# Performance work log

Hardware: AMD Instinct MI355X
Metric: run time of the kernel (lower is better)

Reference implementation:

```python
import jax, jax.numpy as jnp
import numpy as np

NUM_HEADS = 16

def _rmsnorm(x, w):
    eps = jnp.finfo(x.dtype).eps  # torch nn.RMSNorm default eps
    ms = jnp.mean(x * x, axis=-1, keepdims=True)
    return x * jax.lax.rsqrt(ms + eps) * w

def _heads(x):
    B, S, D = x.shape
    return x.reshape(B, S, NUM_HEADS, D // NUM_HEADS)

def _attn(q, k, v):
    # q:[B,Sq,H,D] k,v:[B,Sk,H,D]; non-causal softmax attention
    scale = 1.0 / np.sqrt(q.shape[-1]).astype(np.float32)
    s = jnp.einsum('bqhd,bkhd->bhqk', q, k) * scale
    p = jax.nn.softmax(s, axis=-1)
    return jnp.einsum('bhqk,bkhd->bqhd', p, v)

def _gate(ctx, W1, b1, W2, b2):
    # Linear -> SiLU -> Linear(dim->1) -> sigmoid ; returns [B,S,1]
    h = jax.nn.silu(ctx @ W1.T + b1)
    return jax.nn.sigmoid(h @ W2.T + b2)

def setup_inputs() -> dict:
    key = jax.random.key(0)
    ks = jax.random.split(key, 20)
    B, Sq, Sk, St, dim = 4, 512, 2048, 512, 1024
    n = lambda k, shp, s=1.0: jax.random.normal(k, shp, jnp.float32) * s
    W = lambda k, o, i: n(k, (o, i), 0.02)
    return {
        'queries': n(ks[0], (B, Sq, dim)),
        'context_visual': n(ks[1], (B, Sk, dim)),
        'context_text': n(ks[2], (B, St, dim)),
        'w_norm_q': jnp.ones((dim,), jnp.float32),
        'w_norm_v': jnp.ones((dim,), jnp.float32),
        'w_norm_t': jnp.ones((dim,), jnp.float32),
        'Wq': W(ks[3], dim, dim), 'bq': n(ks[4], (dim,), 0.02),
        'Wk_vis': W(ks[5], dim, dim), 'bk_vis': jnp.zeros((dim,), jnp.float32),
        'Wv_vis': W(ks[6], dim, dim), 'bv_vis': jnp.zeros((dim,), jnp.float32),
        'Wk_text': W(ks[7], dim, dim), 'bk_text': jnp.zeros((dim,), jnp.float32),
        'Wv_text': W(ks[8], dim, dim), 'bv_text': jnp.zeros((dim,), jnp.float32),
        'Wg1v': W(ks[9], dim, dim), 'bg1v': jnp.zeros((dim,), jnp.float32),
        'Wg2v': W(ks[10], 1, dim), 'bg2v': jnp.zeros((1,), jnp.float32),
        'Wg1t': W(ks[11], dim, dim), 'bg1t': jnp.zeros((dim,), jnp.float32),
        'Wg2t': W(ks[12], 1, dim), 'bg2t': jnp.zeros((1,), jnp.float32),
        'Wo': W(ks[13], dim, dim), 'bo': jnp.zeros((dim,), jnp.float32),
    }

def reference(queries, context_visual, context_text,
              w_norm_q, w_norm_v, w_norm_t,
              Wq, bq, Wk_vis, bk_vis, Wv_vis, bv_vis,
              Wk_text, bk_text, Wv_text, bv_text,
              Wg1v, bg1v, Wg2v, bg2v, Wg1t, bg1t, Wg2t, bg2t,
              Wo, bo):
    residual = queries
    qn = _rmsnorm(queries, w_norm_q)
    cv = _rmsnorm(context_visual, w_norm_v)
    ct = _rmsnorm(context_text, w_norm_t)
    q = _heads(qn @ Wq.T + bq)
    k_vis = _heads(cv @ Wk_vis.T + bk_vis)
    v_vis = _heads(cv @ Wv_vis.T + bv_vis)
    v_vis = v_vis * _gate(cv, Wg1v, bg1v, Wg2v, bg2v)[..., None]  # [B,Sk,1,1]
    h = _attn(q, k_vis, v_vis)
    k_text = _heads(ct @ Wk_text.T + bk_text)
    v_text = _heads(ct @ Wv_text.T + bv_text)
    v_text = v_text * _gate(ct, Wg1t, bg1t, Wg2t, bg2t)[..., None]
    h = h + _attn(q, k_text, v_text)
    B, Sq, H, D = h.shape
    out = h.reshape(B, Sq, H * D) @ Wo.T + bo  # dropout p=0 -> identity
    return residual + out
```

## Files before the change

kernel.cpp:

```cpp
#include <hip/hip_runtime.h>
#include <hip/hip_bf16.h>

typedef __attribute__((ext_vector_type(4))) float f32x4;
typedef __attribute__((ext_vector_type(8))) short s16x8;
typedef __attribute__((ext_vector_type(4))) short s16x4;
using bf16 = __hip_bfloat16;

static constexpr int BB  = 4;
static constexpr int SQ  = 512;
static constexpr int SKV = 2048;
static constexpr int SKT = 512;
static constexpr int DIM = 1024;
static constexpr int NH  = 16;
static constexpr int HD  = 64;

#define MFMA32(A,B,C) __builtin_amdgcn_mfma_f32_16x16x32_bf16(A,B,C,0,0,0)

#if __has_builtin(__builtin_amdgcn_mfma_f32_16x16x16_bf16)
  #define MFMA16(A,B,C) __builtin_amdgcn_mfma_f32_16x16x16_bf16(A,B,C,0,0,0)
  #define HAVE_X16 1
#elif __has_builtin(__builtin_amdgcn_mfma_f32_16x16x16bf16_1k)
  #define MFMA16(A,B,C) __builtin_amdgcn_mfma_f32_16x16x16bf16_1k(A,B,C,0,0,0)
  #define HAVE_X16 1
#else
  #define HAVE_X16 0
#endif

#define SBAR() asm volatile("s_barrier" ::: "memory")

__device__ __forceinline__ float b2f(short s) {
  unsigned int u = ((unsigned int)(unsigned short)s) << 16;
  float f; __builtin_memcpy(&f, &u, 4); return f;
}
__device__ __forceinline__ short f2s(float f) {
  bf16 h = __float2bfloat16(f); short s; __builtin_memcpy(&s, &h, 2); return s;
}

__device__ __forceinline__ void gload16(const void* g, void* l) {
  __builtin_amdgcn_global_load_lds(
      (const __attribute__((address_space(1))) void*)g,
      (__attribute__((address_space(3))) void*)l, 16, 0, 0);
}

static constexpr float QSCALE = 0.180336880111120426f;

struct CastArgs { const float* src[10]; bf16* dst[10]; int n[10]; };
__global__ __launch_bounds__(256) void cast_kernel(CastArgs a) {
  const int y = blockIdx.y;
  const int n = a.n[y];
  const int i = (blockIdx.x * 256 + threadIdx.x) * 4;
  if (i >= n) return;
  const float4 v = *(const float4*)(a.src[y] + i);
  bf16* d = a.dst[y] + i;
  d[0] = __float2bfloat16(v.x); d[1] = __float2bfloat16(v.y);
  d[2] = __float2bfloat16(v.z); d[3] = __float2bfloat16(v.w);
}

struct NormArgs { const float* x[3]; const float* w[3]; bf16* y[3]; int rows[3]; };
__global__ __launch_bounds__(256) void rmsnorm_kernel(NormArgs a) {
  const int t = blockIdx.y, row = blockIdx.x;
  if (row >= a.rows[t]) return;
  const float* x = a.x[t] + (size_t)row * DIM;
  const float4 v = *(const float4*)(x + threadIdx.x * 4);
  float ss = v.x*v.x + v.y*v.y + v.z*v.z + v.w*v.w;
  #pragma unroll
  for (int m = 32; m >= 1; m >>= 1) ss += __shfl_xor(ss, m);
  __shared__ float red[4];
  if ((threadIdx.x & 63) == 0) red[threadIdx.x >> 6] = ss;
  __syncthreads();
  ss = red[0] + red[1] + red[2] + red[3];
  const float sc = rsqrtf(ss * (1.0f / DIM) + 1.1920928955078125e-07f);
  const float4 w = *(const float4*)(a.w[t] + threadIdx.x * 4);
  bf16* y = a.y[t] + (size_t)row * DIM + threadIdx.x * 4;
  y[0] = __float2bfloat16(v.x * sc * w.x);
  y[1] = __float2bfloat16(v.y * sc * w.y);
  y[2] = __float2bfloat16(v.z * sc * w.z);
  y[3] = __float2bfloat16(v.w * sc * w.w);
}

struct PSlot { const bf16* A; const bf16* W; const float* bias;
               bf16* Cb; int epi; int sksh; };
struct PArgs { PSlot s[7]; };

__global__ __launch_bounds__(512, 2) void proj256(PArgs a) {
  __shared__ char lds[131072];
  const int tid = threadIdx.x, lane = tid & 63, wave = tid >> 6;
  const int m16 = lane & 15, g16 = lane >> 4;
  const int wm = wave >> 2, wn = wave & 3;

  const int i = (blockIdx.x & 7) * 64 + (blockIdx.x >> 3);
  int slot, rem;
  if (i < 384) { slot = i >> 7; rem = i & 127; }
  else { const int j = i - 384; slot = 3 + (j >> 5); rem = j & 31; }
  const PSlot S = a.s[slot];
  const int bn = rem & 3, bm = rem >> 2;

  const bf16* Ab = S.A + (size_t)bm * 256 * DIM;
  const bf16* Wb = S.W + (size_t)bn * 256 * DIM;

  auto stageA = [&](int k0, int buf) {
    #pragma unroll
    for (int q = 0; q < 4; ++q) {
      const int idx = q * 512 + tid;
      const int row = idx >> 3, g = (idx & 7) ^ (row & 7);
      gload16(Ab + (size_t)row * DIM + k0 + g * 8,
              &lds[buf * 65536 + q * 8192 + wave * 1024]);
    }
  };
  auto stageB = [&](int k0, int buf) {
    #pragma unroll
    for (int q = 0; q < 4; ++q) {
      const int idx = q * 512 + tid;
      const int row = idx >> 3, g = (idx & 7) ^ (row & 7);
      gload16(Wb + (size_t)row * DIM + k0 + g * 8,
              &lds[buf * 65536 + 32768 + q * 8192 + wave * 1024]);
    }
  };

  f32x4 acc[8][4];
  #pragma unroll
  for (int x = 0; x < 8; ++x)
    #pragma unroll
    for (int y = 0; y < 4; ++y)
      #pragma unroll
      for (int r = 0; r < 4; ++r) acc[x][y][r] = 0.0f;

  stageA(0, 0); stageB(0, 0);
  asm volatile("s_waitcnt vmcnt(0)" ::: "memory");
  SBAR();

  for (int t = 0; t < DIM / 64; ++t) {
    const int buf = t & 1;
    const char* A0 = &lds[buf * 65536];
    const char* B0 = A0 + 32768;
    s16x8 af[4][2], bf0[2][2], bf1[2][2];

    #pragma unroll
    for (int mi = 0; mi < 4; ++mi) {
      const int row = wm * 128 + mi * 16 + m16;
      #pragma unroll
      for (int ks = 0; ks < 2; ++ks)
        af[mi][ks] = *(const s16x8*)(A0 + row * 128 + (((ks*4+g16) ^ (m16 & 7)) * 16));
    }
    #pragma unroll
    for (int ni = 0; ni < 2; ++ni) {
      const int row = wn * 64 + ni * 16 + m16;
      #pragma unroll
      for (int ks = 0; ks < 2; ++ks)
        bf0[ni][ks] = *(const s16x8*)(B0 + row * 128 + (((ks*4+g16) ^ (m16 & 7)) * 16));
    }
    if (t + 1 < DIM / 64) stageA((t + 1) * 64, buf ^ 1);
    SBAR();
    __builtin_amdgcn_s_setprio(1);
    #pragma unroll
    for (int mi = 0; mi < 4; ++mi)
      #pragma unroll
      for (int ni = 0; ni < 2; ++ni) {
        acc[mi][ni] = MFMA32(af[mi][0], bf0[ni][0], acc[mi][ni]);
        acc[mi][ni] = MFMA32(af[mi][1], bf0[ni][1], acc[mi][ni]);
      }
    __builtin_amdgcn_s_setprio(0);
    SBAR();

    #pragma unroll
    for (int ni = 0; ni < 2; ++ni) {
      const int row = wn * 64 + 32 + ni * 16 + m16;
      #pragma unroll
      for (int ks = 0; ks < 2; ++ks)
        bf1[ni][ks] = *(const s16x8*)(B0 + row * 128 + (((ks*4+g16) ^ (m16 & 7)) * 16));
    }
    if (t + 1 < DIM / 64) stageB((t + 1) * 64, buf ^ 1);
    SBAR();
    __builtin_amdgcn_s_setprio(1);
    #pragma unroll
    for (int mi = 0; mi < 4; ++mi)
      #pragma unroll
      for (int ni = 0; ni < 2; ++ni) {
        acc[mi][2+ni] = MFMA32(af[mi][0], bf1[ni][0], acc[mi][2+ni]);
        acc[mi][2+ni] = MFMA32(af[mi][1], bf1[ni][1], acc[mi][2+ni]);
      }
    __builtin_amdgcn_s_setprio(0);
    SBAR();

    #pragma unroll
    for (int mi = 0; mi < 4; ++mi) {
      const int row = wm * 128 + 64 + mi * 16 + m16;
      #pragma unroll
      for (int ks = 0; ks < 2; ++ks)
        af[mi][ks] = *(const s16x8*)(A0 + row * 128 + (((ks*4+g16) ^ (m16 & 7)) * 16));
    }
    SBAR();
    __builtin_amdgcn_s_setprio(1);
    #pragma unroll
    for (int mi = 0; mi < 4; ++mi)
      #pragma unroll
      for (int ni = 0; ni < 2; ++ni) {
        acc[4+mi][ni] = MFMA32(af[mi][0], bf0[ni][0], acc[4+mi][ni]);
        acc[4+mi][ni] = MFMA32(af[mi][1], bf0[ni][1], acc[4+mi][ni]);
      }
    __builtin_amdgcn_s_setprio(0);
    SBAR();

    __builtin_amdgcn_s_setprio(1);
    #pragma unroll
    for (int mi = 0; mi < 4; ++mi)
      #pragma unroll
      for (int ni = 0; ni < 2; ++ni) {
        acc[4+mi][2+ni] = MFMA32(af[mi][0], bf1[ni][0], acc[4+mi][2+ni]);
        acc[4+mi][2+ni] = MFMA32(af[mi][1], bf1[ni][1], acc[4+mi][2+ni]);
      }
    __builtin_amdgcn_s_setprio(0);
    asm volatile("s_waitcnt vmcnt(0) lgkmcnt(0)" ::: "memory");
    SBAR();
  }

  const int r0 = bm * 256 + wm * 128, c0 = bn * 256 + wn * 64;
  if (S.epi >= 3) {
    const float sc = (S.epi == 3) ? QSCALE : 1.0f;
    const int msk = (1 << S.sksh) - 1;
    #pragma unroll
    for (int ng = 0; ng < 4; ++ng) {
      const int col = c0 + ng * 16 + m16;
      const int hh = col >> 6, d = col & 63;
      const float bv = S.bias[col];
      #pragma unroll
      for (int mg = 0; mg < 8; ++mg) {
        const int rowb = r0 + mg * 16 + g16 * 4;
        #pragma unroll
        for (int r = 0; r < 4; ++r) {
          const int m = rowb + r;
          const int bb2 = m >> S.sksh, tok = m & msk;
          S.Cb[(((size_t)(bb2 * NH + hh) << S.sksh) + tok) * HD + d] =
              __float2bfloat16((acc[mg][ng][r] + bv) * sc);
        }
      }
    }
  } else {
    #pragma unroll
    for (int ng = 0; ng < 4; ++ng) {
      const int col = c0 + ng * 16 + m16;
      const float bv = S.bias[col];
      #pragma unroll
      for (int mg = 0; mg < 8; ++mg) {
        const int rowb = r0 + mg * 16 + g16 * 4;
        #pragma unroll
        for (int r = 0; r < 4; ++r) {
          float v = acc[mg][ng][r] + bv;
          const size_t idx = (size_t)(rowb + r) * DIM + col;
          if (S.epi == 1) { v = v / (1.0f + __expf(-v)); S.Cb[idx] = __float2bfloat16(v); }
          else            { S.Cb[idx] = __float2bfloat16(v); }
        }
      }
    }
  }
}

struct GSlot { const bf16* A; const bf16* W; const float* bias;
               const float* resid; float* Cf; };
__global__ __launch_bounds__(256) void gemm_sb(GSlot S) {
  constexpr int K = DIM;
  __shared__ alignas(16) char sA[8192];
  __shared__ alignas(16) char sB[8192];
  const int tid = threadIdx.x, lane = tid & 63, wave = tid >> 6;
  const int bm = blockIdx.x, bn = blockIdx.y;
  const int wm = wave >> 1, wn = wave & 1;
  const int m16 = lane & 15, g16 = lane >> 4;

  f32x4 acc[4][4];
  #pragma unroll
  for (int i = 0; i < 4; ++i)
    #pragma unroll
    for (int j = 0; j < 4; ++j)
      #pragma unroll
      for (int r = 0; r < 4; ++r) acc[i][j][r] = 0.0f;

  const bf16* Ab = S.A + (size_t)bm * 128 * K;
  const bf16* Wb = S.W + (size_t)bn * 128 * K;

  for (int t = 0; t < K / 32; ++t) {
    const int k0 = t * 32;
    #pragma unroll
    for (int p = 0; p < 2; ++p) {
      const int idx = p * 256 + tid;
      const int row = idx >> 2, sg = (idx & 3) ^ (row & 3);
      const size_t so = (size_t)row * K + k0 + sg * 8;
      gload16(Ab + so, &sA[p * 4096 + wave * 1024]);
      gload16(Wb + so, &sB[p * 4096 + wave * 1024]);
    }
    __syncthreads();
    s16x8 af[4], bfr[4];
    #pragma unroll
    for (int mi = 0; mi < 4; ++mi) {
      const int row = wm * 64 + mi * 16 + m16;
      af[mi] = *(const s16x8*)(&sA[row * 64 + (g16 ^ (m16 & 3)) * 16]);
    }
    #pragma unroll
    for (int ni = 0; ni < 4; ++ni) {
      const int row = wn * 64 + ni * 16 + m16;
      bfr[ni] = *(const s16x8*)(&sB[row * 64 + (g16 ^ (m16 & 3)) * 16]);
    }
    #pragma unroll
    for (int mi = 0; mi < 4; ++mi)
      #pragma unroll
      for (int ni = 0; ni < 4; ++ni)
        acc[mi][ni] = MFMA32(af[mi], bfr[ni], acc[mi][ni]);
    __syncthreads();
  }

  const int r0 = bm * 128 + wm * 64, c0 = bn * 128 + wn * 64;
  #pragma unroll
  for (int ni = 0; ni < 4; ++ni) {
    const int col = c0 + ni * 16 + m16;
    const float bv = S.bias[col];
    #pragma unroll
    for (int mi = 0; mi < 4; ++mi) {
      const int rowb = r0 + mi * 16 + g16 * 4;
      #pragma unroll
      for (int r = 0; r < 4; ++r) {
        const size_t idx = (size_t)(rowb + r) * DIM + col;
        S.Cf[idx] = acc[mi][ni][r] + bv + S.resid[idx];
      }
    }
  }
}

__global__ __launch_bounds__(256) void gate2_kernel(
    const bf16* __restrict__ g1v, const bf16* __restrict__ w2v,
    const float* __restrict__ b2v, float* __restrict__ gv,
    const bf16* __restrict__ g1t, const bf16* __restrict__ w2t,
    const float* __restrict__ b2t, float* __restrict__ gt)
{
  const int lane = threadIdx.x & 63, wave = threadIdx.x >> 6;
  int row = blockIdx.x * 4 + wave;
  const bf16* x; const bf16* w2; const float* b2; float* gate;
  if (row < BB * SKV) { x = g1v + (size_t)row * DIM; w2 = w2v; b2 = b2v; gate = gv + row; }
  else { row -= BB * SKV; x = g1t + (size_t)row * DIM; w2 = w2t; b2 = b2t; gate = gt + row; }
  float sum = 0.0f;
  #pragma unroll
  for (int c = 0; c < 2; ++c) {
    const int i0 = c * 512 + lane * 8;
    const s16x8 xv = *(const s16x8*)(x + i0);
    const s16x8 wv = *(const s16x8*)(w2 + i0);
    #pragma unroll
    for (int j = 0; j < 8; ++j) sum += b2f(xv[j]) * b2f(wv[j]);
  }
  #pragma unroll
  for (int m = 32; m >= 1; m >>= 1) sum += __shfl_xor(sum, m);
  if (lane == 0) *gate = 1.0f / (1.0f + __expf(-(sum + b2[0])));
}

__global__ __launch_bounds__(256) void vtrans2_kernel(
    const bf16* __restrict__ Vv, const float* __restrict__ gv, bf16* __restrict__ VTv,
    const bf16* __restrict__ Vt, const float* __restrict__ gt, bf16* __restrict__ VTt)
{
  __shared__ alignas(16) short tile[64][72];
  int kt = blockIdx.x;
  const bf16* V; const float* gate; bf16* VT; int Sk;
  if (kt < SKV / 64) { V = Vv; gate = gv; VT = VTv; Sk = SKV; }
  else { kt -= SKV / 64; V = Vt; gate = gt; VT = VTt; Sk = SKT; }
  const int h = blockIdx.y, b = blockIdx.z;
  const int tid = threadIdx.x;
  #pragma unroll
  for (int i = 0; i < 2; ++i) {
    const int c = tid + i * 256;
    const int kr = c >> 3, d0 = (c & 7) * 8;
    const float g = gate[(size_t)b * Sk + kt * 64 + kr];
    const s16x8 v = *(const s16x8*)(V + ((size_t)(b*Sk + kt*64 + kr)*NH + h)*HD + d0);
    #pragma unroll
    for (int j = 0; j < 8; ++j) tile[kr][d0 + j] = f2s(b2f(v[j]) * g);
  }
  __syncthreads();
  #pragma unroll
  for (int i = 0; i < 2; ++i) {
    const int c = tid + i * 256;
    const int d = c >> 3, k0 = (c & 7) * 8;
    s16x8 v;
    #pragma unroll
    for (int j = 0; j < 8; ++j) v[j] = tile[k0 + j][d];
    *(s16x8*)(VT + ((size_t)(b*NH + h)*HD + d)*Sk + kt*64 + k0) = v;
  }
}

__global__ __launch_bounds__(256, 4) void attn_kernel(
    const bf16* __restrict__ Qh,
    const bf16* __restrict__ K1h, const bf16* __restrict__ VT1,
    const bf16* __restrict__ K2h, const bf16* __restrict__ VT2,
    bf16* __restrict__ Hout)
{
  __shared__ alignas(16) char sK[2][8192];
  __shared__ alignas(16) char sVT[2][8192];
  const int tid = threadIdx.x, lane = tid & 63, wave = tid >> 6;
  const int hb = blockIdx.x;
  const int h = hb & 15, b = hb >> 4;
  const int wq = wave & 1, hf = wave >> 1;
  const int q0 = blockIdx.y * 32 + wq * 16;
  const int m16 = lane & 15, g16 = lane >> 4;

  const bf16* qrow = Qh + ((size_t)(b*NH + h)*SQ + q0 + m16)*HD;
  const s16x8 qf0 = *(const s16x8*)(qrow + g16 * 8);
  const s16x8 qf1 = *(const s16x8*)(qrow + 32 + g16 * 8);

  const bf16* K1b  = K1h + (size_t)(b*NH + h) * SKV * HD;
  const bf16* K2b  = K2h + (size_t)(b*NH + h) * SKT * HD;
  const bf16* VT1b = VT1 + (size_t)(b*NH + h) * HD * SKV;
  const bf16* VT2b = VT2 + (size_t)(b*NH + h) * HD * SKT;

  auto stage = [&](const bf16* Kb, const bf16* VTb, int Sk, int b0, int b1) {
    #pragma unroll
    for (int p = 0; p < 2; ++p) {
      const int idx = p * 256 + tid;
      const int r = idx >> 3, g = (idx & 7) ^ (r & 7);
      gload16(Kb  + (size_t)(b0 + r) * HD + g * 8, &sK[0][p * 4096 + wave * 1024]);
      gload16(Kb  + (size_t)(b1 + r) * HD + g * 8, &sK[1][p * 4096 + wave * 1024]);
      gload16(VTb + (size_t)r * Sk + b0 + g * 8,   &sVT[0][p * 4096 + wave * 1024]);
      gload16(VTb + (size_t)r * Sk + b1 + g * 8,   &sVT[1][p * 4096 + wave * 1024]);
    }
  };

  float of[4][4];
  #pragma unroll
  for (int i = 0; i < 4; ++i)
    #pragma unroll
    for (int r = 0; r < 4; ++r) of[i][r] = 0.0f;

  f32x4 o[4];
  float mx, l;
  auto reset_state = [&]() {
    #pragma unroll
    for (int i = 0; i < 4; ++i)
      #pragma unroll
      for (int r = 0; r < 4; ++r) o[i][r] = 0.0f;
    mx = -1e30f; l = 0.0f;
  };

  auto chunk = [&]() {
    const char* kbase = &sK[hf][0];
    const char* vbase = &sVT[hf][0];
    f32x4 s[4];
    #pragma unroll
    for (int nt = 0; nt < 4; ++nt) {
      const char* kr = kbase + (nt * 16 + m16) * 128;
      const s16x8 kf0 = *(const s16x8*)(kr + ((g16    ) ^ (m16 & 7)) * 16);
      const s16x8 kf1 = *(const s16x8*)(kr + ((4 + g16) ^ (m16 & 7)) * 16);
      f32x4 a2; a2[0] = 0; a2[1] = 0; a2[2] = 0; a2[3] = 0;
      a2 = MFMA32(kf0, qf0, a2);
      a2 = MFMA32(kf1, qf1, a2);
      s[nt] = a2;
    }
    float mc = s[0][0];
    #pragma unroll
    for (int nt = 0; nt < 4; ++nt)
      #pragma unroll
      for (int r = 0; r < 4; ++r) mc = fmaxf(mc, s[nt][r]);
    mc = fmaxf(mc, __shfl_xor(mc, 16));
    mc = fmaxf(mc, __shfl_xor(mc, 32));
    const float mnew = fmaxf(mx, mc);
    const float alpha = exp2f(mx - mnew);
    mx = mnew;
    float p[4][4]; float rs = 0.0f;
    #pragma unroll
    for (int nt = 0; nt < 4; ++nt)
      #pragma unroll
      for (int r = 0; r < 4; ++r) { p[nt][r] = exp2f(s[nt][r] - mnew); rs += p[nt][r]; }
    rs += __shfl_xor(rs, 16);
    rs += __shfl_xor(rs, 32);
    l = l * alpha + rs;
    float av[4];
    #pragma unroll
    for (int r = 0; r < 4; ++r) av[r] = __shfl(alpha, g16 * 4 + r);
    #pragma unroll
    for (int nd = 0; nd < 4; ++nd)
      #pragma unroll
      for (int r = 0; r < 4; ++r) o[nd][r] *= av[r];
#if HAVE_X16
    #pragma unroll
    for (int nt = 0; nt < 4; ++nt) {
      s16x4 pa;
      pa[0] = f2s(p[nt][0]); pa[1] = f2s(p[nt][1]);
      pa[2] = f2s(p[nt][2]); pa[3] = f2s(p[nt][3]);
      #pragma unroll
      for (int nd = 0; nd < 4; ++nd) {
        const int d = nd * 16 + m16;
        const int g = (nt * 2 + (g16 >> 1)) ^ (m16 & 7);
        const s16x4 vf = *(const s16x4*)(vbase + d * 128 + g * 16 + (g16 & 1) * 8);
        o[nd] = MFMA16(pa, vf, o[nd]);
      }
    }
#endif
  };

  auto merge_flush = [&]() {
    __syncthreads();
    float* mo = (float*)&sK[0][0];
    float* ml = (float*)&sVT[0][0];
    if (hf) {
      #pragma unroll
      for (int nd = 0; nd < 4; ++nd)
        #pragma unroll
        for (int r = 0; r < 4; ++r)
          mo[(wq * 16 + g16 * 4 + r) * 64 + nd * 16 + m16] = o[nd][r];
      if (g16 == 0) { ml[(wq * 2 + 0) * 16 + m16] = mx; ml[(wq * 2 + 1) * 16 + m16] = l; }
    }
    __syncthreads();
    if (!hf) {
      const float mb = ml[(wq * 2 + 0) * 16 + m16];
      const float lb = ml[(wq * 2 + 1) * 16 + m16];
      const float ms = fmaxf(mx, mb);
      const float aA = exp2f(mx - ms), aB = exp2f(mb - ms);
      const float lt = l * aA + lb * aB;
      float aAv[4], aBv[4], ltv[4];
      #pragma unroll
      for (int r = 0; r < 4; ++r) {
        aAv[r] = __shfl(aA, g16 * 4 + r);
        aBv[r] = __shfl(aB, g16 * 4 + r);
        ltv[r] = __shfl(lt, g16 * 4 + r);
      }
      #pragma unroll
      for (int nd = 0; nd < 4; ++nd)
        #pragma unroll
        for (int r = 0; r < 4; ++r) {
          const float ob = mo[(wq * 16 + g16 * 4 + r) * 64 + nd * 16 + m16];
          of[nd][r] += (o[nd][r] * aAv[r] + ob * aBv[r]) / ltv[r];
        }
    }
    __syncthreads();
  };

  reset_state();
  for (int c = 0; c < SKV / 128; ++c) {
    stage(K1b, VT1b, SKV, c * 64, 1024 + c * 64);
    __syncthreads();
    chunk();
    __syncthreads();
  }
  merge_flush();

  reset_state();
  for (int c = 0; c < SKT / 128; ++c) {
    stage(K2b, VT2b, SKT, c * 64, 256 + c * 64);
    __syncthreads();
    chunk();
    __syncthreads();
  }
  merge_flush();

  if (!hf) {
    #pragma unroll
    for (int nd = 0; nd < 4; ++nd)
      #pragma unroll
      for (int r = 0; r < 4; ++r) {
        const int row = q0 + g16 * 4 + r;
        Hout[((size_t)(b*SQ + row)*NH + h)*HD + nd*16 + m16] =
            __float2bfloat16(of[nd][r]);
      }
  }
}

extern "C" void kernel_launch(void* const* d_in, const int* in_sizes, int n_in,
                              void* d_out, int out_size, void* d_ws, size_t ws_size,
                              hipStream_t stream)
{
  const float* queries = (const float*)d_in[0];
  const float* ctx_v   = (const float*)d_in[1];
  const float* ctx_t   = (const float*)d_in[2];
  const float* w_nq = (const float*)d_in[3];
  const float* w_nv = (const float*)d_in[4];
  const float* w_nt = (const float*)d_in[5];
  const float* Wq   = (const float*)d_in[6];  const float* bq   = (const float*)d_in[7];
  const float* Wk_v = (const float*)d_in[8];  const float* bk_v = (const float*)d_in[9];
  const float* Wv_v = (const float*)d_in[10]; const float* bv_v = (const float*)d_in[11];
  const float* Wk_t = (const float*)d_in[12]; const float* bk_t = (const float*)d_in[13];
  const float* Wv_t = (const float*)d_in[14]; const float* bv_t = (const float*)d_in[15];
  const float* Wg1v = (const float*)d_in[16]; const float* bg1v = (const float*)d_in[17];
  const float* Wg2v = (const float*)d_in[18]; const float* bg2v = (const float*)d_in[19];
  const float* Wg1t = (const float*)d_in[20]; const float* bg1t = (const float*)d_in[21];
  const float* Wg2t = (const float*)d_in[22]; const float* bg2t = (const float*)d_in[23];
  const float* Wo   = (const float*)d_in[24]; const float* bo   = (const float*)d_in[25];

  char* ws = (char*)d_ws;
  size_t off = 0;
  auto alloc = [&](size_t n) { void* p = ws + off; off += (n + 255) & ~(size_t)255; return p; };

  const size_t MATB = (size_t)DIM * DIM * 2;
  bf16* WqB   = (bf16*)alloc(MATB);
  bf16* WkvB  = (bf16*)alloc(MATB);
  bf16* WvvB  = (bf16*)alloc(MATB);
  bf16* WktB  = (bf16*)alloc(MATB);
  bf16* WvtB  = (bf16*)alloc(MATB);
  bf16* Wg1vB = (bf16*)alloc(MATB);
  bf16* Wg1tB = (bf16*)alloc(MATB);
  bf16* WoB   = (bf16*)alloc(MATB);
  bf16* Wg2vB = (bf16*)alloc(2048);
  bf16* Wg2tB = (bf16*)alloc(2048);

  bf16* qn  = (bf16*)alloc((size_t)BB*SQ*DIM*2);
  bf16* cv  = (bf16*)alloc((size_t)BB*SKV*DIM*2);
  bf16* ct  = (bf16*)alloc((size_t)BB*SKT*DIM*2);
  bf16* qb  = (bf16*)alloc((size_t)BB*SQ*DIM*2);
  bf16* kvB = (bf16*)alloc((size_t)BB*SKV*DIM*2);
  bf16* ktB = (bf16*)alloc((size_t)BB*SKT*DIM*2);
  bf16* vtV = (bf16*)alloc((size_t)BB*SKV*DIM*2);
  bf16* vtT = (bf16*)alloc((size_t)BB*SKT*DIM*2);
  bf16* vScrV = (bf16*)alloc((size_t)BB*SKV*DIM*2);
  bf16* vScrT = (bf16*)alloc((size_t)BB*SKT*DIM*2);
  bf16* g1V   = (bf16*)alloc((size_t)BB*SKV*DIM*2);
  bf16* g1T   = (bf16*)alloc((size_t)BB*SKT*DIM*2);
  float* gateV = (float*)alloc((size_t)BB*SKV*4);
  float* gateT = (float*)alloc((size_t)BB*SKT*4);
  bf16* hB  = (bf16*)alloc((size_t)BB*SQ*DIM*2);
  (void)ws_size; (void)n_in; (void)in_sizes; (void)out_size;

  CastArgs ca;
  const float* wsrc[10] = {Wq, Wk_v, Wv_v, Wk_t, Wv_t, Wg1v, Wg1t, Wo, Wg2v, Wg2t};
  bf16* wdst[10] = {WqB, WkvB, WvvB, WktB, WvtB, Wg1vB, Wg1tB, WoB, Wg2vB, Wg2tB};
  for (int i = 0; i < 10; ++i) {
    ca.src[i] = wsrc[i]; ca.dst[i] = wdst[i];
    ca.n[i] = (i < 8) ? DIM * DIM : DIM;
  }
  cast_kernel<<<dim3(1024, 10), 256, 0, stream>>>(ca);

  NormArgs na;
  na.x[0] = queries; na.x[1] = ctx_v; na.x[2] = ctx_t;
  na.w[0] = w_nq;    na.w[1] = w_nv;  na.w[2] = w_nt;
  na.y[0] = qn;      na.y[1] = cv;    na.y[2] = ct;
  na.rows[0] = BB*SQ; na.rows[1] = BB*SKV; na.rows[2] = BB*SKT;
  rmsnorm_kernel<<<dim3(BB*SKV, 3), 256, 0, stream>>>(na);

  PArgs pa;
  pa.s[0] = {cv, WkvB,  bk_v, kvB,   4, 11};
  pa.s[1] = {cv, WvvB,  bv_v, vScrV, 0, 0};
  pa.s[2] = {cv, Wg1vB, bg1v, g1V,   1, 0};
  pa.s[3] = {qn, WqB,   bq,   qb,    3, 9};
  pa.s[4] = {ct, WktB,  bk_t, ktB,   4, 9};
  pa.s[5] = {ct, WvtB,  bv_t, vScrT, 0, 0};
  pa.s[6] = {ct, Wg1tB, bg1t, g1T,   1, 0};
  proj256<<<dim3(512), 512, 0, stream>>>(pa);

  gate2_kernel<<<dim3((BB*SKV + BB*SKT) / 4), 256, 0, stream>>>(
      g1V, Wg2vB, bg2v, gateV, g1T, Wg2tB, bg2t, gateT);
  vtrans2_kernel<<<dim3(SKV/64 + SKT/64, NH, BB), 256, 0, stream>>>(
      vScrV, gateV, vtV, vScrT, gateT, vtT);

  attn_kernel<<<dim3(NH*BB, SQ/32), 256, 0, stream>>>(qb, kvB, vtV, ktB, vtT, hB);

  GSlot go{hB, WoB, bo, queries, (float*)d_out};
  gemm_sb<<<dim3(BB*SQ/128, 8), 256, 0, stream>>>(go);
}
```

Baseline: 214.0 us.

## Fuse cast and rmsnorm launches, deepen projection prefetch, retile output GEMM

Folds the weight-cast and RMSNorm kernels into one prep launch over a flat grid, removing a kernel launch and the wasted idle blocks of the old 2D norm grid. The projection GEMM now prefetches two K-tiles ahead, issuing loads after each buffer is consumed and waiting with a partial vmcnt instead of draining every iteration, so global loads overlap more with MFMA. The output GEMM moves to 64-row tiles with a 4x2 per-wave layout, doubling its block count to fill more CUs. The trade-off is more complex wait accounting and a smaller per-block tile with less reuse in the output GEMM.

```diff
diff --git a/kernel.cpp b/kernel.cpp
--- a/kernel.cpp
+++ b/kernel.cpp
@@ -44,23 +44,28 @@
 
 static constexpr float QSCALE = 0.180336880111120426f;
 
-struct CastArgs { const float* src[10]; bf16* dst[10]; int n[10]; };
-__global__ __launch_bounds__(256) void cast_kernel(CastArgs a) {
-  const int y = blockIdx.y;
-  const int n = a.n[y];
-  const int i = (blockIdx.x * 256 + threadIdx.x) * 4;
-  if (i >= n) return;
-  const float4 v = *(const float4*)(a.src[y] + i);
-  bf16* d = a.dst[y] + i;
-  d[0] = __float2bfloat16(v.x); d[1] = __float2bfloat16(v.y);
-  d[2] = __float2bfloat16(v.z); d[3] = __float2bfloat16(v.w);
-}
-
-struct NormArgs { const float* x[3]; const float* w[3]; bf16* y[3]; int rows[3]; };
-__global__ __launch_bounds__(256) void rmsnorm_kernel(NormArgs a) {
-  const int t = blockIdx.y, row = blockIdx.x;
-  if (row >= a.rows[t]) return;
-  const float* x = a.x[t] + (size_t)row * DIM;
+struct PrepArgs {
+  const float* csrc[10]; bf16* cdst[10]; int cn[10];
+  const float* nx[3]; const float* nw[3]; bf16* ny[3];
+};
+__global__ __launch_bounds__(256) void prep_kernel(PrepArgs a) {
+  const int bx = blockIdx.x;
+  if (bx < 10240) {
+    const int y = bx >> 10;
+    const int i = ((bx & 1023) * 256 + threadIdx.x) * 4;
+    if (i >= a.cn[y]) return;
+    const float4 v = *(const float4*)(a.csrc[y] + i);
+    bf16* d = a.cdst[y] + i;
+    d[0] = __float2bfloat16(v.x); d[1] = __float2bfloat16(v.y);
+    d[2] = __float2bfloat16(v.z); d[3] = __float2bfloat16(v.w);
+    return;
+  }
+  const int j = bx - 10240;
+  int t, row;
+  if (j < 2048) { t = 0; row = j; }
+  else if (j < 10240) { t = 1; row = j - 2048; }
+  else { t = 2; row = j - 10240; }
+  const float* x = a.nx[t] + (size_t)row * DIM;
   const float4 v = *(const float4*)(x + threadIdx.x * 4);
   float ss = v.x*v.x + v.y*v.y + v.z*v.z + v.w*v.w;
   #pragma unroll
@@ -70,8 +75,8 @@
   __syncthreads();
   ss = red[0] + red[1] + red[2] + red[3];
   const float sc = rsqrtf(ss * (1.0f / DIM) + 1.1920928955078125e-07f);
-  const float4 w = *(const float4*)(a.w[t] + threadIdx.x * 4);
-  bf16* y = a.y[t] + (size_t)row * DIM + threadIdx.x * 4;
+  const float4 w = *(const float4*)(a.nw[t] + threadIdx.x * 4);
+  bf16* y = a.ny[t] + (size_t)row * DIM + threadIdx.x * 4;
   y[0] = __float2bfloat16(v.x * sc * w.x);
   y[1] = __float2bfloat16(v.y * sc * w.y);
   y[2] = __float2bfloat16(v.z * sc * w.z);
@@ -126,10 +131,12 @@
       for (int r = 0; r < 4; ++r) acc[x][y][r] = 0.0f;
 
   stageA(0, 0); stageB(0, 0);
-  asm volatile("s_waitcnt vmcnt(0)" ::: "memory");
+  stageA(64, 1); stageB(64, 1);
+  asm volatile("s_waitcnt vmcnt(8)" ::: "memory");
   SBAR();
 
-  for (int t = 0; t < DIM / 64; ++t) {
+  constexpr int NT = DIM / 64;
+  for (int t = 0; t < NT; ++t) {
     const int buf = t & 1;
     const char* A0 = &lds[buf * 65536];
     const char* B0 = A0 + 32768;
@@ -149,7 +156,6 @@
       for (int ks = 0; ks < 2; ++ks)
         bf0[ni][ks] = *(const s16x8*)(B0 + row * 128 + (((ks*4+g16) ^ (m16 & 7)) * 16));
     }
-    if (t + 1 < DIM / 64) stageA((t + 1) * 64, buf ^ 1);
     SBAR();
     __builtin_amdgcn_s_setprio(1);
     #pragma unroll
@@ -169,7 +175,6 @@
       for (int ks = 0; ks < 2; ++ks)
         bf1[ni][ks] = *(const s16x8*)(B0 + row * 128 + (((ks*4+g16) ^ (m16 & 7)) * 16));
     }
-    if (t + 1 < DIM / 64) stageB((t + 1) * 64, buf ^ 1);
     SBAR();
     __builtin_amdgcn_s_setprio(1);
     #pragma unroll
@@ -182,6 +187,7 @@
     __builtin_amdgcn_s_setprio(0);
     SBAR();
 
+    if (t + 2 < NT) stageB((t + 2) * 64, buf);
     #pragma unroll
     for (int mi = 0; mi < 4; ++mi) {
       const int row = wm * 128 + 64 + mi * 16 + m16;
@@ -201,6 +207,7 @@
     __builtin_amdgcn_s_setprio(0);
     SBAR();
 
+    if (t + 2 < NT) stageA((t + 2) * 64, buf);
     __builtin_amdgcn_s_setprio(1);
     #pragma unroll
     for (int mi = 0; mi < 4; ++mi)
@@ -210,7 +217,8 @@
         acc[4+mi][2+ni] = MFMA32(af[mi][1], bf1[ni][1], acc[4+mi][2+ni]);
       }
     __builtin_amdgcn_s_setprio(0);
-    asm volatile("s_waitcnt vmcnt(0) lgkmcnt(0)" ::: "memory");
+    if (t < NT - 2)       { asm volatile("s_waitcnt vmcnt(8)" ::: "memory"); }
+    else if (t == NT - 2) { asm volatile("s_waitcnt vmcnt(0)" ::: "memory"); }
     SBAR();
   }
 
@@ -257,59 +265,60 @@
 
 struct GSlot { const bf16* A; const bf16* W; const float* bias;
                const float* resid; float* Cf; };
-__global__ __launch_bounds__(256) void gemm_sb(GSlot S) {
+__global__ __launch_bounds__(256) void gemm_out(GSlot S) {
   constexpr int K = DIM;
-  __shared__ alignas(16) char sA[8192];
+  __shared__ alignas(16) char sA[4096];
   __shared__ alignas(16) char sB[8192];
   const int tid = threadIdx.x, lane = tid & 63, wave = tid >> 6;
   const int bm = blockIdx.x, bn = blockIdx.y;
-  const int wm = wave >> 1, wn = wave & 1;
   const int m16 = lane & 15, g16 = lane >> 4;
 
-  f32x4 acc[4][4];
+  f32x4 acc[4][2];
   #pragma unroll
   for (int i = 0; i < 4; ++i)
     #pragma unroll
-    for (int j = 0; j < 4; ++j)
+    for (int j = 0; j < 2; ++j)
       #pragma unroll
       for (int r = 0; r < 4; ++r) acc[i][j][r] = 0.0f;
 
-  const bf16* Ab = S.A + (size_t)bm * 128 * K;
+  const bf16* Ab = S.A + (size_t)bm * 64 * K;
   const bf16* Wb = S.W + (size_t)bn * 128 * K;
 
   for (int t = 0; t < K / 32; ++t) {
     const int k0 = t * 32;
+    {
+      const int row = tid >> 2, sg = (tid & 3) ^ (row & 3);
+      gload16(Ab + (size_t)row * K + k0 + sg * 8, &sA[wave * 1024]);
+    }
     #pragma unroll
     for (int p = 0; p < 2; ++p) {
       const int idx = p * 256 + tid;
       const int row = idx >> 2, sg = (idx & 3) ^ (row & 3);
-      const size_t so = (size_t)row * K + k0 + sg * 8;
-      gload16(Ab + so, &sA[p * 4096 + wave * 1024]);
-      gload16(Wb + so, &sB[p * 4096 + wave * 1024]);
-    }
-    __syncthreads();
-    s16x8 af[4], bfr[4];
+      gload16(Wb + (size_t)row * K + k0 + sg * 8, &sB[p * 4096 + wave * 1024]);
+    }
+    __syncthreads();
+    s16x8 af[4], bfr[2];
     #pragma unroll
     for (int mi = 0; mi < 4; ++mi) {
-      const int row = wm * 64 + mi * 16 + m16;
+      const int row = mi * 16 + m16;
       af[mi] = *(const s16x8*)(&sA[row * 64 + (g16 ^ (m16 & 3)) * 16]);
     }
     #pragma unroll
-    for (int ni = 0; ni < 4; ++ni) {
-      const int row = wn * 64 + ni * 16 + m16;
+    for (int ni = 0; ni < 2; ++ni) {
+      const int row = wave * 32 + ni * 16 + m16;
       bfr[ni] = *(const s16x8*)(&sB[row * 64 + (g16 ^ (m16 & 3)) * 16]);
     }
     #pragma unroll
     for (int mi = 0; mi < 4; ++mi)
       #pragma unroll
-      for (int ni = 0; ni < 4; ++ni)
+      for (int ni = 0; ni < 2; ++ni)
         acc[mi][ni] = MFMA32(af[mi], bfr[ni], acc[mi][ni]);
     __syncthreads();
   }
 
-  const int r0 = bm * 128 + wm * 64, c0 = bn * 128 + wn * 64;
-  #pragma unroll
-  for (int ni = 0; ni < 4; ++ni) {
+  const int r0 = bm * 64, c0 = bn * 128 + wave * 32;
+  #pragma unroll
+  for (int ni = 0; ni < 2; ++ni) {
     const int col = c0 + ni * 16 + m16;
     const float bv = S.bias[col];
     #pragma unroll
@@ -610,21 +619,17 @@
   bf16* hB  = (bf16*)alloc((size_t)BB*SQ*DIM*2);
   (void)ws_size; (void)n_in; (void)in_sizes; (void)out_size;
 
-  CastArgs ca;
+  PrepArgs pr;
   const float* wsrc[10] = {Wq, Wk_v, Wv_v, Wk_t, Wv_t, Wg1v, Wg1t, Wo, Wg2v, Wg2t};
   bf16* wdst[10] = {WqB, WkvB, WvvB, WktB, WvtB, Wg1vB, Wg1tB, WoB, Wg2vB, Wg2tB};
   for (int i = 0; i < 10; ++i) {
-    ca.src[i] = wsrc[i]; ca.dst[i] = wdst[i];
-    ca.n[i] = (i < 8) ? DIM * DIM : DIM;
-  }
-  cast_kernel<<<dim3(1024, 10), 256, 0, stream>>>(ca);
-
-  NormArgs na;
-  na.x[0] = queries; na.x[1] = ctx_v; na.x[2] = ctx_t;
-  na.w[0] = w_nq;    na.w[1] = w_nv;  na.w[2] = w_nt;
-  na.y[0] = qn;      na.y[1] = cv;    na.y[2] = ct;
-  na.rows[0] = BB*SQ; na.rows[1] = BB*SKV; na.rows[2] = BB*SKT;
-  rmsnorm_kernel<<<dim3(BB*SKV, 3), 256, 0, stream>>>(na);
+    pr.csrc[i] = wsrc[i]; pr.cdst[i] = wdst[i];
+    pr.cn[i] = (i < 8) ? DIM * DIM : DIM;
+  }
+  pr.nx[0] = queries; pr.nx[1] = ctx_v; pr.nx[2] = ctx_t;
+  pr.nw[0] = w_nq;    pr.nw[1] = w_nv;  pr.nw[2] = w_nt;
+  pr.ny[0] = qn;      pr.ny[1] = cv;    pr.ny[2] = ct;
+  prep_kernel<<<dim3(10240 + 12288), 256, 0, stream>>>(pr);
 
   PArgs pa;
   pa.s[0] = {cv, WkvB,  bk_v, kvB,   4, 11};
@@ -644,5 +649,5 @@
   attn_kernel<<<dim3(NH*BB, SQ/32), 256, 0, stream>>>(qb, kvB, vtV, ktB, vtT, hB);
 
   GSlot go{hB, WoB, bo, queries, (float*)d_out};
-  gemm_sb<<<dim3(BB*SQ/128, 8), 256, 0, stream>>>(go);
-}
+  gemm_out<<<dim3(BB*SQ/64, 8), 256, 0, stream>>>(go);
+}
```

Result: faster. 203.4 us (-5.0%).
